# Optimization experiments

Measured on AMD Instinct MI355X. Metric: run time of the kernel, lower is better.

The kernel has to match this reference:

```python
import jax, jax.numpy as jnp
import numpy as np

B, CTX, QST, E, H = 8, 4096, 512, 300, 128

def setup_inputs() -> dict:
    key = jax.random.key(0)
    k1, k2, k3, k4 = jax.random.split(key, 4)
    context_sequence = jax.random.normal(k1, (B, CTX, E), dtype=jnp.float32)
    question_sequence = jax.random.normal(k2, (B, QST, E), dtype=jnp.float32)
    question_mask = jnp.ones((B, QST), dtype=jnp.int32)
    # dense layer params (PyTorch Linear: y = x @ W.T + b)
    bound = 1.0 / np.sqrt(E)
    W = jax.random.uniform(k3, (H, E), minval=-bound, maxval=bound, dtype=jnp.float32)
    b = jax.random.uniform(k4, (H,), minval=-bound, maxval=bound, dtype=jnp.float32)
    return {"context_sequence": context_sequence, "question_sequence": question_sequence,
            "question_mask": question_mask, "W": W, "b": b}

def reference(context_sequence, question_sequence, question_mask, W, b):
    # ReLU(dense(x)) for both sequences
    ctx_logits = jax.nn.relu(jnp.einsum('bce,he->bch', context_sequence, W) + b)   # [B, CTX, H]
    qst_logits = jax.nn.relu(jnp.einsum('bqe,he->bqh', question_sequence, W) + b)  # [B, QST, H]
    scores = jnp.einsum('bch,bqh->bcq', ctx_logits, qst_logits)                    # [B, CTX, QST]
    scores = jnp.where(question_mask[:, None, :] == 0, -jnp.inf, scores)
    attn = jax.nn.softmax(scores, axis=-1)
    return jnp.einsum('bcq,bqh->bch', attn, qst_logits)                            # [B, CTX, H]
```

## Files before the change

kernel.cpp:

```cpp
#include <hip/hip_runtime.h>
#include <hip/hip_bf16.h>

#define BB   8
#define SCTX 4096
#define SQ   512
#define EE   300
#define HH   128
#define EP   320
#define CST  328
#define LOG2E 1.4426950408889634f

typedef short bhalf4 __attribute__((ext_vector_type(4)));
typedef short short8 __attribute__((ext_vector_type(8)));
typedef float f32x4  __attribute__((ext_vector_type(4)));
typedef unsigned u32x4 __attribute__((ext_vector_type(4)));

#define MFMA16(a, b, c) __builtin_amdgcn_mfma_f32_16x16x32_bf16((a), (b), (c), 0, 0, 0)

__device__ __forceinline__ short f2bf(float f) {
  unsigned u = __builtin_bit_cast(unsigned, f);
  u += 0x7fffu + ((u >> 16) & 1u);
  return (short)(u >> 16);
}
__device__ __forceinline__ float bf2f(short s) {
  return __builtin_bit_cast(float, ((unsigned)(unsigned short)s) << 16);
}
__device__ __forceinline__ unsigned pack2(float a, float b) {
  return (unsigned)(unsigned short)f2bf(a) | ((unsigned)(unsigned short)f2bf(b) << 16);
}
__device__ __forceinline__ void gload16(const void* g, void* lds) {
  __builtin_amdgcn_global_load_lds(
      (const __attribute__((address_space(1))) void*)g,
      (__attribute__((address_space(3))) void*)lds, 16, 0, 0);
}

__global__ void k_wpad(const float* __restrict__ W, short* __restrict__ wsw) {
  const int h = blockIdx.x, k = threadIdx.x;
  float v = (k < EE) ? W[h * EE + k] : 0.0f;
  const int m = h >> 4, t = h & 15, kk = k >> 5, quad = (k >> 3) & 3, j = k & 7;
  wsw[((kk * 8 + m) * 64 + quad * 16 + t) * 8 + j] = f2bf(v);
}

__global__ __launch_bounds__(256) void k_qlog(const float* __restrict__ qst,
                                              const short* __restrict__ wsw,
                                              const float* __restrict__ bias,
                                              short* __restrict__ ql,
                                              short* __restrict__ qlT) {
  const int b = blockIdx.y;
  const int m0 = blockIdx.x * 32;
  const int tid = threadIdx.x;
  const int w = tid >> 6, l = tid & 63, t = l & 15, quad = l >> 4;
  const int g = w >> 1, hf = w & 1;

  __shared__ __align__(16) short cst[32 * CST];

  const float4* cbase = (const float4*)(qst + (size_t)(b * SQ + m0) * EE);
#pragma unroll
  for (int j = 0; j < 10; ++j) {
    int i4 = tid + j * 256;
    if (i4 < 2400) {
      float4 v = cbase[i4];
      int row = i4 / 75, c4 = i4 - row * 75;
      bhalf4 s4; s4[0] = f2bf(v.x); s4[1] = f2bf(v.y); s4[2] = f2bf(v.z); s4[3] = f2bf(v.w);
      *(bhalf4*)(cst + row * CST + c4 * 4) = s4;
    }
  }
  for (int i = tid; i < 320; i += 256) {
    int row = i / 10, c = (i - row * 10) * 2;
    *(int*)&cst[row * CST + 300 + c] = 0;
  }
  __syncthreads();

  const short* arow = cst + (g * 16 + t) * CST;
  f32x4 acc[4] = {};
#pragma unroll
  for (int kk = 0; kk < 10; ++kk) {
    const int k = kk * 32 + quad * 8;
    short8 a = *(const short8*)(arow + k);
    short8 w8[4];
#pragma unroll
    for (int n = 0; n < 4; ++n)
      w8[n] = *(const short8*)(wsw + ((kk * 8 + hf * 4 + n) * 64 + l) * 8);
#pragma unroll
    for (int n = 0; n < 4; ++n) acc[n] = MFMA16(a, w8[n], acc[n]);
  }
#pragma unroll
  for (int n = 0; n < 4; ++n) {
    const int h = (hf * 4 + n) * 16 + t;
    const float bv = bias[h];
    bhalf4 s4;
#pragma unroll
    for (int r = 0; r < 4; ++r) {
      float v = fmaxf(acc[n][r] + bv, 0.0f);
      short s16 = f2bf(v);
      s4[r] = s16;
      const int row = m0 + g * 16 + quad * 4 + r;
      ql[((size_t)b * SQ + row) * HH + h] = s16;
    }
    *(bhalf4*)&qlT[((size_t)b * HH + h) * SQ + m0 + g * 16 + quad * 4] = s4;
  }
}

__global__ __launch_bounds__(256, 2) void k_attn(const float* __restrict__ ctx,
                                                 const short* __restrict__ wsw,
                                                 const float* __restrict__ bias,
                                                 const int* __restrict__ mask,
                                                 const short* __restrict__ ql,
                                                 const short* __restrict__ qlT,
                                                 float* __restrict__ out) {
  const int b = blockIdx.y;
  const int m0 = blockIdx.x * 64;
  const int tid = threadIdx.x;
  const int w = tid >> 6, l = tid & 63, t = l & 15, quad = l >> 4;
  const int g = w >> 1, hf = w & 1;

  __shared__ __align__(16) short uq[16384];
  __shared__ __align__(16) short uv[16384];
  __shared__ short maskh[SQ];
  short* cst = uq;
  short* qch = uq;
  short* clt = uv;
  short* vch = uv;

  for (int i = tid; i < SQ; i += 256)
    maskh[i] = f2bf(mask[b * SQ + i] ? -8.0f : -1e30f);

  for (int i = 0; i < 2; ++i) {
    const float4* cbase = (const float4*)(ctx + ((size_t)b * SCTX + m0 + i * 32) * EE);
#pragma unroll
    for (int j = 0; j < 10; ++j) {
      int i4 = tid + j * 256;
      if (i4 < 2400) {
        float4 v = cbase[i4];
        int row = i4 / 75, c4 = i4 - row * 75;
        bhalf4 s4; s4[0] = f2bf(v.x); s4[1] = f2bf(v.y); s4[2] = f2bf(v.z); s4[3] = f2bf(v.w);
        *(bhalf4*)(cst + row * CST + c4 * 4) = s4;
      }
    }
    for (int k = tid; k < 320; k += 256) {
      int row = k / 10, c = (k - row * 10) * 2;
      *(int*)&cst[row * CST + 300 + c] = 0;
    }
    __syncthreads();
    const short* arow = cst + (g * 16 + t) * CST;
    f32x4 acc[4] = {};
#pragma unroll
    for (int kk = 0; kk < 10; ++kk) {
      const int k = kk * 32 + quad * 8;
      short8 a = *(const short8*)(arow + k);
      short8 w8[4];
#pragma unroll
      for (int n = 0; n < 4; ++n)
        w8[n] = *(const short8*)(wsw + ((kk * 8 + hf * 4 + n) * 64 + l) * 8);
#pragma unroll
      for (int n = 0; n < 4; ++n) acc[n] = MFMA16(a, w8[n], acc[n]);
    }
#pragma unroll
    for (int n = 0; n < 4; ++n) {
      const int h = (hf * 4 + n) * 16 + t;
      const float bv = bias[h];
#pragma unroll
      for (int r = 0; r < 4; ++r) {
        float v = fmaxf(acc[n][r] + bv, 0.0f);
        clt[(i * 32 + g * 16 + quad * 4 + r) * 136 + h] = f2bf(v);
      }
    }
    __syncthreads();
  }

  short8 af[4];
#pragma unroll
  for (int kk = 0; kk < 4; ++kk)
    af[kk] = *(const short8*)&clt[(w * 16 + t) * 136 + kk * 32 + quad * 8];

  const int srcA = ((quad & 1) * 2) * 16 + t;
  const int srcB = srcA + 16;
  const bool hiq = quad >= 2;
  const int sx = (t & 7) << 3;
  const int rl = l >> 4;
  const int cb = (l & 15) * 16;

  auto stageQ = [&](int c) {
#pragma unroll
    for (int s = 0; s < 8; ++s) {
      const int row = w * 32 + s * 4 + rl;
      const int sw = cb ^ ((row & 7) << 4);
      gload16((const char*)(ql + ((size_t)b * SQ + c * 128 + row) * HH) + sw,
              qch + (w * 32 + s * 4) * 128);
    }
  };
  auto stageV = [&](int c) {
#pragma unroll
    for (int s = 0; s < 8; ++s) {
      const int row = w * 32 + s * 4 + rl;
      const int sw = cb ^ ((row & 7) << 4);
      gload16((const char*)(qlT + ((size_t)b * HH + row) * SQ + c * 128) + sw,
              vch + (w * 32 + s * 4) * 128);
    }
  };

  stageQ(0);

  f32x4 o[8] = {};
  float rtot = 0.0f;
  for (int c = 0; c < 4; ++c) {
    __syncthreads();
    stageV(c);

    f32x4 sv[8] = {};
#pragma unroll
    for (int kk = 0; kk < 4; ++kk) {
      const short* qrE = qch + ((kk * 2) * 16 + t) * 128;
      const short* qrO = qrE + 16 * 128;
#pragma unroll
      for (int kx = 0; kx < 4; ++kx) {
        const int co = (kx * 32 + quad * 8) ^ sx;
        sv[kk * 2]     = MFMA16(*(const short8*)(qrE + co), af[kx], sv[kk * 2]);
        sv[kk * 2 + 1] = MFMA16(*(const short8*)(qrO + co), af[kx], sv[kk * 2 + 1]);
      }
    }
    unsigned pk[16];
#pragma unroll
    for (int kk = 0; kk < 4; ++kk) {
      bhalf4 mbE = *(const bhalf4*)&maskh[c * 128 + (kk * 2) * 16 + quad * 4];
      bhalf4 mbO = *(const bhalf4*)&maskh[c * 128 + (kk * 2 + 1) * 16 + quad * 4];
      float pE[4], pO[4];
#pragma unroll
      for (int r = 0; r < 4; ++r) {
        pE[r] = exp2f((sv[kk * 2][r] + bf2f(mbE[r])) * LOG2E);
        pO[r] = exp2f((sv[kk * 2 + 1][r] + bf2f(mbO[r])) * LOG2E);
        rtot += pE[r] + pO[r];
      }
      pk[kk * 4 + 0] = pack2(pE[0], pE[1]);
      pk[kk * 4 + 1] = pack2(pE[2], pE[3]);
      pk[kk * 4 + 2] = pack2(pO[0], pO[1]);
      pk[kk * 4 + 3] = pack2(pO[2], pO[3]);
    }
    unsigned sA[16], sB[16];
#pragma unroll
    for (int i = 0; i < 16; ++i) {
      sA[i] = (unsigned)__shfl((int)pk[i], srcA);
      sB[i] = (unsigned)__shfl((int)pk[i], srcB);
    }

    __syncthreads();

    if (c < 3) stageQ(c + 1);

#pragma unroll
    for (int kk = 0; kk < 4; ++kk) {
      u32x4 av;
      av[0] = hiq ? sA[kk * 4 + 2] : sA[kk * 4 + 0];
      av[1] = hiq ? sA[kk * 4 + 3] : sA[kk * 4 + 1];
      av[2] = hiq ? sB[kk * 4 + 2] : sB[kk * 4 + 0];
      av[3] = hiq ? sB[kk * 4 + 3] : sB[kk * 4 + 1];
      short8 pa = __builtin_bit_cast(short8, av);
      const int co = (kk * 32 + quad * 8) ^ sx;
#pragma unroll
      for (int n = 0; n < 8; ++n) {
        short8 v8 = *(const short8*)&vch[(n * 16 + t) * 128 + co];
        o[n] = MFMA16(pa, v8, o[n]);
      }
    }
  }

  rtot += __shfl_xor(rtot, 16);
  rtot += __shfl_xor(rtot, 32);
  f32x4 rinv;
#pragma unroll
  for (int r = 0; r < 4; ++r) rinv[r] = 1.0f / __shfl(rtot, quad * 4 + r);
  float* obase = out + ((size_t)b * SCTX + m0 + w * 16) * HH;
#pragma unroll
  for (int n = 0; n < 8; ++n)
#pragma unroll
    for (int r = 0; r < 4; ++r)
      obase[(quad * 4 + r) * HH + n * 16 + t] = o[n][r] * rinv[r];
}

extern "C" void kernel_launch(void* const* d_in, const int* in_sizes, int n_in,
                              void* d_out, int out_size, void* d_ws, size_t ws_size,
                              hipStream_t stream) {
  const float* ctx  = (const float*)d_in[0];
  const float* qst  = (const float*)d_in[1];
  const int*   mask = (const int*)d_in[2];
  const float* W    = (const float*)d_in[3];
  const float* bias = (const float*)d_in[4];
  float* out = (float*)d_out;

  short* wsw  = (short*)d_ws;
  short* ql   = (short*)((char*)d_ws + 81920);
  short* qlT  = ql + (size_t)BB * SQ * HH;

  k_wpad<<<dim3(HH), dim3(EP), 0, stream>>>(W, wsw);
  k_qlog<<<dim3(SQ / 32, BB), dim3(256), 0, stream>>>(qst, wsw, bias, ql, qlT);
  k_attn<<<dim3(SCTX / 64, BB), dim3(256), 0, stream>>>(ctx, wsw, bias, mask, ql, qlT, out);
}
```

Measured before the change: 121.1 us.

## Halve attention tile to 32 rows and split question keys across warps

```diff
diff --git a/kernel.cpp b/kernel.cpp
--- a/kernel.cpp
+++ b/kernel.cpp
@@ -8,6 +8,7 @@
 #define HH   128
 #define EP   320
 #define CST  328
+#define CSH  168
 #define LOG2E 1.4426950408889634f
 
 typedef short bhalf4 __attribute__((ext_vector_type(4)));
@@ -109,172 +110,193 @@
                                                  const short* __restrict__ qlT,
                                                  float* __restrict__ out) {
   const int b = blockIdx.y;
-  const int m0 = blockIdx.x * 64;
+  const int m0 = blockIdx.x * 32;
   const int tid = threadIdx.x;
   const int w = tid >> 6, l = tid & 63, t = l & 15, quad = l >> 4;
-  const int g = w >> 1, hf = w & 1;
-
-  __shared__ __align__(16) short uq[16384];
-  __shared__ __align__(16) short uv[16384];
-  __shared__ short maskh[SQ];
-  short* cst = uq;
+  const int rg = w & 1, qh = w >> 1;
+
+  __shared__ __align__(16) short uq[8192];
+  __shared__ __align__(16) short uv[8192];
+  __shared__ __align__(16) short maskh[SQ];
   short* qch = uq;
-  short* clt = uv;
+  short* csth = uv;
   short* vch = uv;
+
+  const int rl4 = l >> 4;
+  const int cbq = (l & 15) * 16;
+  const int rl8 = l >> 3;
+  const int cbv = (l & 7) * 16;
+
+  auto stageQ = [&](int c) {
+#pragma unroll
+    for (int s = 0; s < 4; ++s) {
+      const int row = w * 16 + s * 4 + rl4;
+      gload16((const char*)(ql + ((size_t)b * SQ + c * 64 + row) * HH) +
+                  (cbq ^ ((row & 7) << 4)),
+              qch + (w * 16 + s * 4) * 128);
+    }
+  };
+  auto stageV = [&](int c) {
+#pragma unroll
+    for (int s = 0; s < 4; ++s) {
+      const int row = w * 32 + s * 8 + rl8;
+      gload16((const char*)(qlT + ((size_t)b * HH + row) * SQ + c * 64) +
+                  (cbv ^ ((row & 7) << 4)),
+              vch + (w * 32 + s * 8) * 64);
+    }
+  };
+
+  stageQ(0);
 
   for (int i = tid; i < SQ; i += 256)
     maskh[i] = f2bf(mask[b * SQ + i] ? -8.0f : -1e30f);
 
-  for (int i = 0; i < 2; ++i) {
-    const float4* cbase = (const float4*)(ctx + ((size_t)b * SCTX + m0 + i * 32) * EE);
-#pragma unroll
-    for (int j = 0; j < 10; ++j) {
-      int i4 = tid + j * 256;
-      if (i4 < 2400) {
-        float4 v = cbase[i4];
-        int row = i4 / 75, c4 = i4 - row * 75;
+  f32x4 acc[8] = {};
+  for (int kh = 0; kh < 2; ++kh) {
+    if (kh == 0) {
+#pragma unroll
+      for (int j = 0; j < 5; ++j) {
+        int i4 = tid + j * 256;
+        int row = i4 / 40, c4 = i4 - row * 40;
+        float4 v = *(const float4*)(ctx + ((size_t)b * SCTX + m0 + row) * EE + c4 * 4);
         bhalf4 s4; s4[0] = f2bf(v.x); s4[1] = f2bf(v.y); s4[2] = f2bf(v.z); s4[3] = f2bf(v.w);
-        *(bhalf4*)(cst + row * CST + c4 * 4) = s4;
-      }
-    }
-    for (int k = tid; k < 320; k += 256) {
-      int row = k / 10, c = (k - row * 10) * 2;
-      *(int*)&cst[row * CST + 300 + c] = 0;
+        *(bhalf4*)(csth + row * CSH + c4 * 4) = s4;
+      }
+    } else {
+#pragma unroll
+      for (int j = 0; j < 5; ++j) {
+        int i4 = tid + j * 256;
+        if (i4 < 1120) {
+          int row = i4 / 35, c4 = i4 - row * 35;
+          float4 v = *(const float4*)(ctx + ((size_t)b * SCTX + m0 + row) * EE + 160 + c4 * 4);
+          bhalf4 s4; s4[0] = f2bf(v.x); s4[1] = f2bf(v.y); s4[2] = f2bf(v.z); s4[3] = f2bf(v.w);
+          *(bhalf4*)(csth + row * CSH + c4 * 4) = s4;
+        }
+      }
+      for (int i = tid; i < 320; i += 256) {
+        int row = i / 10, ci = (i - row * 10) * 2;
+        *(int*)&csth[row * CSH + 140 + ci] = 0;
+      }
     }
     __syncthreads();
-    const short* arow = cst + (g * 16 + t) * CST;
-    f32x4 acc[4] = {};
-#pragma unroll
-    for (int kk = 0; kk < 10; ++kk) {
-      const int k = kk * 32 + quad * 8;
-      short8 a = *(const short8*)(arow + k);
-      short8 w8[4];
-#pragma unroll
-      for (int n = 0; n < 4; ++n)
-        w8[n] = *(const short8*)(wsw + ((kk * 8 + hf * 4 + n) * 64 + l) * 8);
-#pragma unroll
-      for (int n = 0; n < 4; ++n) acc[n] = MFMA16(a, w8[n], acc[n]);
-    }
-#pragma unroll
-    for (int n = 0; n < 4; ++n) {
-      const int h = (hf * 4 + n) * 16 + t;
-      const float bv = bias[h];
-#pragma unroll
-      for (int r = 0; r < 4; ++r) {
-        float v = fmaxf(acc[n][r] + bv, 0.0f);
-        clt[(i * 32 + g * 16 + quad * 4 + r) * 136 + h] = f2bf(v);
+    const short* arow = csth + (rg * 16 + t) * CSH;
+#pragma unroll
+    for (int kkl = 0; kkl < 5; ++kkl) {
+      const int kk = kh * 5 + kkl;
+      short8 a = *(const short8*)(arow + kkl * 32 + quad * 8);
+#pragma unroll
+      for (int n = 0; n < 8; ++n) {
+        short8 w8 = *(const short8*)(wsw + ((kk * 8 + n) * 64 + l) * 8);
+        acc[n] = MFMA16(w8, a, acc[n]);
       }
     }
     __syncthreads();
   }
-
-  short8 af[4];
-#pragma unroll
-  for (int kk = 0; kk < 4; ++kk)
-    af[kk] = *(const short8*)&clt[(w * 16 + t) * 136 + kk * 32 + quad * 8];
 
   const int srcA = ((quad & 1) * 2) * 16 + t;
   const int srcB = srcA + 16;
   const bool hiq = quad >= 2;
+  unsigned pkA[8][2];
+#pragma unroll
+  for (int n = 0; n < 8; ++n) {
+    float4 bv = *(const float4*)(bias + n * 16 + quad * 4);
+    pkA[n][0] = pack2(fmaxf(acc[n][0] + bv.x, 0.f), fmaxf(acc[n][1] + bv.y, 0.f));
+    pkA[n][1] = pack2(fmaxf(acc[n][2] + bv.z, 0.f), fmaxf(acc[n][3] + bv.w, 0.f));
+  }
+  short8 af[4];
+#pragma unroll
+  for (int kk = 0; kk < 4; ++kk) {
+    unsigned e0 = (unsigned)__shfl((int)pkA[kk * 2][0], srcA);
+    unsigned e1 = (unsigned)__shfl((int)pkA[kk * 2][1], srcA);
+    unsigned e2 = (unsigned)__shfl((int)pkA[kk * 2][0], srcB);
+    unsigned e3 = (unsigned)__shfl((int)pkA[kk * 2][1], srcB);
+    unsigned o0 = (unsigned)__shfl((int)pkA[kk * 2 + 1][0], srcA);
+    unsigned o1 = (unsigned)__shfl((int)pkA[kk * 2 + 1][1], srcA);
+    unsigned o2 = (unsigned)__shfl((int)pkA[kk * 2 + 1][0], srcB);
+    unsigned o3 = (unsigned)__shfl((int)pkA[kk * 2 + 1][1], srcB);
+    u32x4 a4;
+    a4[0] = hiq ? o0 : e0;
+    a4[1] = hiq ? o1 : e1;
+    a4[2] = hiq ? o2 : e2;
+    a4[3] = hiq ? o3 : e3;
+    af[kk] = __builtin_bit_cast(short8, a4);
+  }
+
   const int sx = (t & 7) << 3;
-  const int rl = l >> 4;
-  const int cb = (l & 15) * 16;
-
-  auto stageQ = [&](int c) {
-#pragma unroll
-    for (int s = 0; s < 8; ++s) {
-      const int row = w * 32 + s * 4 + rl;
-      const int sw = cb ^ ((row & 7) << 4);
-      gload16((const char*)(ql + ((size_t)b * SQ + c * 128 + row) * HH) + sw,
-              qch + (w * 32 + s * 4) * 128);
-    }
-  };
-  auto stageV = [&](int c) {
-#pragma unroll
-    for (int s = 0; s < 8; ++s) {
-      const int row = w * 32 + s * 4 + rl;
-      const int sw = cb ^ ((row & 7) << 4);
-      gload16((const char*)(qlT + ((size_t)b * HH + row) * SQ + c * 128) + sw,
-              vch + (w * 32 + s * 4) * 128);
-    }
-  };
-
-  stageQ(0);
-
   f32x4 o[8] = {};
   float rtot = 0.0f;
-  for (int c = 0; c < 4; ++c) {
+  for (int c = 0; c < 8; ++c) {
     __syncthreads();
     stageV(c);
-
-    f32x4 sv[8] = {};
-#pragma unroll
-    for (int kk = 0; kk < 4; ++kk) {
-      const short* qrE = qch + ((kk * 2) * 16 + t) * 128;
-      const short* qrO = qrE + 16 * 128;
+    f32x4 sv[2] = {};
+#pragma unroll
+    for (int n2 = 0; n2 < 2; ++n2) {
+      const short* qr = qch + (qh * 32 + n2 * 16 + t) * 128;
 #pragma unroll
       for (int kx = 0; kx < 4; ++kx) {
-        const int co = (kx * 32 + quad * 8) ^ sx;
-        sv[kk * 2]     = MFMA16(*(const short8*)(qrE + co), af[kx], sv[kk * 2]);
-        sv[kk * 2 + 1] = MFMA16(*(const short8*)(qrO + co), af[kx], sv[kk * 2 + 1]);
-      }
-    }
-    unsigned pk[16];
-#pragma unroll
-    for (int kk = 0; kk < 4; ++kk) {
-      bhalf4 mbE = *(const bhalf4*)&maskh[c * 128 + (kk * 2) * 16 + quad * 4];
-      bhalf4 mbO = *(const bhalf4*)&maskh[c * 128 + (kk * 2 + 1) * 16 + quad * 4];
-      float pE[4], pO[4];
-#pragma unroll
-      for (int r = 0; r < 4; ++r) {
-        pE[r] = exp2f((sv[kk * 2][r] + bf2f(mbE[r])) * LOG2E);
-        pO[r] = exp2f((sv[kk * 2 + 1][r] + bf2f(mbO[r])) * LOG2E);
-        rtot += pE[r] + pO[r];
-      }
-      pk[kk * 4 + 0] = pack2(pE[0], pE[1]);
-      pk[kk * 4 + 1] = pack2(pE[2], pE[3]);
-      pk[kk * 4 + 2] = pack2(pO[0], pO[1]);
-      pk[kk * 4 + 3] = pack2(pO[2], pO[3]);
-    }
-    unsigned sA[16], sB[16];
-#pragma unroll
-    for (int i = 0; i < 16; ++i) {
+        short8 b8 = *(const short8*)(qr + ((kx * 32 + quad * 8) ^ sx));
+        sv[n2] = MFMA16(b8, af[kx], sv[n2]);
+      }
+    }
+    unsigned pk[4];
+#pragma unroll
+    for (int n2 = 0; n2 < 2; ++n2) {
+      bhalf4 mb = *(const bhalf4*)&maskh[c * 64 + qh * 32 + n2 * 16 + quad * 4];
+      float p0 = exp2f((sv[n2][0] + bf2f(mb[0])) * LOG2E);
+      float p1 = exp2f((sv[n2][1] + bf2f(mb[1])) * LOG2E);
+      float p2 = exp2f((sv[n2][2] + bf2f(mb[2])) * LOG2E);
+      float p3 = exp2f((sv[n2][3] + bf2f(mb[3])) * LOG2E);
+      rtot += (p0 + p1) + (p2 + p3);
+      pk[n2 * 2 + 0] = pack2(p0, p1);
+      pk[n2 * 2 + 1] = pack2(p2, p3);
+    }
+    unsigned sA[4], sB[4];
+#pragma unroll
+    for (int i = 0; i < 4; ++i) {
       sA[i] = (unsigned)__shfl((int)pk[i], srcA);
       sB[i] = (unsigned)__shfl((int)pk[i], srcB);
     }
-
     __syncthreads();
-
-    if (c < 3) stageQ(c + 1);
-
-#pragma unroll
-    for (int kk = 0; kk < 4; ++kk) {
-      u32x4 av;
-      av[0] = hiq ? sA[kk * 4 + 2] : sA[kk * 4 + 0];
-      av[1] = hiq ? sA[kk * 4 + 3] : sA[kk * 4 + 1];
-      av[2] = hiq ? sB[kk * 4 + 2] : sB[kk * 4 + 0];
-      av[3] = hiq ? sB[kk * 4 + 3] : sB[kk * 4 + 1];
-      short8 pa = __builtin_bit_cast(short8, av);
-      const int co = (kk * 32 + quad * 8) ^ sx;
-#pragma unroll
-      for (int n = 0; n < 8; ++n) {
-        short8 v8 = *(const short8*)&vch[(n * 16 + t) * 128 + co];
-        o[n] = MFMA16(pa, v8, o[n]);
-      }
-    }
-  }
-
-  rtot += __shfl_xor(rtot, 16);
-  rtot += __shfl_xor(rtot, 32);
-  f32x4 rinv;
-#pragma unroll
-  for (int r = 0; r < 4; ++r) rinv[r] = 1.0f / __shfl(rtot, quad * 4 + r);
-  float* obase = out + ((size_t)b * SCTX + m0 + w * 16) * HH;
-#pragma unroll
-  for (int n = 0; n < 8; ++n)
-#pragma unroll
-    for (int r = 0; r < 4; ++r)
-      obase[(quad * 4 + r) * HH + n * 16 + t] = o[n][r] * rinv[r];
+    if (c < 7) stageQ(c + 1);
+    u32x4 av;
+    av[0] = hiq ? sA[2] : sA[0];
+    av[1] = hiq ? sA[3] : sA[1];
+    av[2] = hiq ? sB[2] : sB[0];
+    av[3] = hiq ? sB[3] : sB[1];
+    short8 pa = __builtin_bit_cast(short8, av);
+#pragma unroll
+    for (int n = 0; n < 8; ++n) {
+      short8 v8 = *(const short8*)&vch[(n * 16 + t) * 64 + ((qh * 32 + quad * 8) ^ sx)];
+      o[n] = MFMA16(pa, v8, o[n]);
+    }
+  }
+
+  float* obuf = (float*)uq;
+  float* rbuf = (float*)maskh;
+  if (qh == 1) {
+#pragma unroll
+    for (int n = 0; n < 8; ++n)
+      *(f32x4*)&obuf[rg * 2048 + n * 256 + l * 4] = o[n];
+    rbuf[rg * 64 + l] = rtot;
+  }
+  __syncthreads();
+  if (qh == 0) {
+    rtot += rbuf[rg * 64 + l];
+#pragma unroll
+    for (int n = 0; n < 8; ++n)
+      o[n] += *(const f32x4*)&obuf[rg * 2048 + n * 256 + l * 4];
+    rtot += __shfl_xor(rtot, 16);
+    rtot += __shfl_xor(rtot, 32);
+    f32x4 rinv;
+#pragma unroll
+    for (int r = 0; r < 4; ++r) rinv[r] = 1.0f / __shfl(rtot, quad * 4 + r);
+    float* obase = out + ((size_t)b * SCTX + m0 + rg * 16) * HH;
+#pragma unroll
+    for (int n = 0; n < 8; ++n)
+#pragma unroll
+      for (int r = 0; r < 4; ++r)
+        obase[(quad * 4 + r) * HH + n * 16 + t] = o[n][r] * rinv[r];
+  }
 }
 
 extern "C" void kernel_launch(void* const* d_in, const int* in_sizes, int n_in,
@@ -293,5 +315,5 @@
 
   k_wpad<<<dim3(HH), dim3(EP), 0, stream>>>(W, wsw);
   k_qlog<<<dim3(SQ / 32, BB), dim3(256), 0, stream>>>(qst, wsw, bias, ql, qlT);
-  k_attn<<<dim3(SCTX / 64, BB), dim3(256), 0, stream>>>(ctx, wsw, bias, mask, ql, qlT, out);
-}
+  k_attn<<<dim3(SCTX / 32, BB), dim3(256), 0, stream>>>(ctx, wsw, bias, mask, ql, qlT, out);
+}
```

Result: slower. 131.6 us (+8.7%).

## Double-buffer Q and V chunks with 64-wide tiles and manual vmcnt waits

Applied to the files above, without the earlier changes.

```diff
diff --git a/kernel.cpp b/kernel.cpp
--- a/kernel.cpp
+++ b/kernel.cpp
@@ -16,6 +16,8 @@
 typedef unsigned u32x4 __attribute__((ext_vector_type(4)));
 
 #define MFMA16(a, b, c) __builtin_amdgcn_mfma_f32_16x16x32_bf16((a), (b), (c), 0, 0, 0)
+#define SBAR()   __builtin_amdgcn_s_barrier()
+#define SCHED0() __builtin_amdgcn_sched_barrier(0)
 
 __device__ __forceinline__ short f2bf(float f) {
   unsigned u = __builtin_bit_cast(unsigned, f);
@@ -116,11 +118,11 @@
 
   __shared__ __align__(16) short uq[16384];
   __shared__ __align__(16) short uv[16384];
-  __shared__ short maskh[SQ];
+  __shared__ __align__(16) short maskh[SQ];
   short* cst = uq;
-  short* qch = uq;
   short* clt = uv;
-  short* vch = uv;
+  short* qb0 = uq;          short* qb1 = uq + 8192;
+  short* vb0 = uv;          short* vb1 = uv + 8192;
 
   for (int i = tid; i < SQ; i += 256)
     maskh[i] = f2bf(mask[b * SQ + i] ? -8.0f : -1e30f);
@@ -172,95 +174,93 @@
 #pragma unroll
   for (int kk = 0; kk < 4; ++kk)
     af[kk] = *(const short8*)&clt[(w * 16 + t) * 136 + kk * 32 + quad * 8];
+  __syncthreads();
 
   const int srcA = ((quad & 1) * 2) * 16 + t;
   const int srcB = srcA + 16;
   const bool hiq = quad >= 2;
-  const int sx = (t & 7) << 3;
-  const int rl = l >> 4;
-  const int cb = (l & 15) * 16;
-
-  auto stageQ = [&](int c) {
-#pragma unroll
-    for (int s = 0; s < 8; ++s) {
-      const int row = w * 32 + s * 4 + rl;
-      const int sw = cb ^ ((row & 7) << 4);
-      gload16((const char*)(ql + ((size_t)b * SQ + c * 128 + row) * HH) + sw,
-              qch + (w * 32 + s * 4) * 128);
+  const int sx  = (t & 7) << 3;
+  const int rl4 = l >> 4;
+  const int cbq = (l & 15) * 16;
+  const int rl8 = l >> 3;
+  const int cbv = (l & 7) * 16;
+
+  auto stageTo = [&](short* qb, short* vb, int c) {
+#pragma unroll
+    for (int s = 0; s < 4; ++s) {
+      const int row = w * 16 + s * 4 + rl4;
+      gload16((const char*)(ql + ((size_t)b * SQ + c * 64 + row) * HH) +
+                  (cbq ^ ((row & 7) << 4)),
+              qb + (w * 16 + s * 4) * 128);
+    }
+#pragma unroll
+    for (int s = 0; s < 4; ++s) {
+      const int row = w * 32 + s * 8 + rl8;
+      gload16((const char*)(qlT + ((size_t)b * HH + row) * SQ + c * 64) +
+                  (cbv ^ ((row & 7) << 4)),
+              vb + (w * 32 + s * 8) * 64);
     }
   };
-  auto stageV = [&](int c) {
-#pragma unroll
-    for (int s = 0; s < 8; ++s) {
-      const int row = w * 32 + s * 4 + rl;
-      const int sw = cb ^ ((row & 7) << 4);
-      gload16((const char*)(qlT + ((size_t)b * HH + row) * SQ + c * 128) + sw,
-              vch + (w * 32 + s * 4) * 128);
-    }
-  };
-
-  stageQ(0);
+
+  stageTo(qb0, vb0, 0);
+  stageTo(qb1, vb1, 1);
 
   f32x4 o[8] = {};
   float rtot = 0.0f;
-  for (int c = 0; c < 4; ++c) {
-    __syncthreads();
-    stageV(c);
-
-    f32x4 sv[8] = {};
-#pragma unroll
-    for (int kk = 0; kk < 4; ++kk) {
-      const short* qrE = qch + ((kk * 2) * 16 + t) * 128;
-      const short* qrO = qrE + 16 * 128;
+  for (int c = 0; c < 8; ++c) {
+    short* qch = (c & 1) ? qb1 : qb0;
+    short* vch = (c & 1) ? vb1 : vb0;
+    if (c < 7) { asm volatile("s_waitcnt vmcnt(8)" ::: "memory"); }
+    else       { asm volatile("s_waitcnt vmcnt(0)" ::: "memory"); }
+    SCHED0(); SBAR(); SCHED0();
+
+    f32x4 sv[4] = {};
+#pragma unroll
+    for (int n2 = 0; n2 < 4; ++n2) {
+      const short* qr = qch + (n2 * 16 + t) * 128;
 #pragma unroll
       for (int kx = 0; kx < 4; ++kx) {
-        const int co = (kx * 32 + quad * 8) ^ sx;
-        sv[kk * 2]     = MFMA16(*(const short8*)(qrE + co), af[kx], sv[kk * 2]);
-        sv[kk * 2 + 1] = MFMA16(*(const short8*)(qrO + co), af[kx], sv[kk * 2 + 1]);
-      }
-    }
-    unsigned pk[16];
-#pragma unroll
-    for (int kk = 0; kk < 4; ++kk) {
-      bhalf4 mbE = *(const bhalf4*)&maskh[c * 128 + (kk * 2) * 16 + quad * 4];
-      bhalf4 mbO = *(const bhalf4*)&maskh[c * 128 + (kk * 2 + 1) * 16 + quad * 4];
-      float pE[4], pO[4];
-#pragma unroll
-      for (int r = 0; r < 4; ++r) {
-        pE[r] = exp2f((sv[kk * 2][r] + bf2f(mbE[r])) * LOG2E);
-        pO[r] = exp2f((sv[kk * 2 + 1][r] + bf2f(mbO[r])) * LOG2E);
-        rtot += pE[r] + pO[r];
-      }
-      pk[kk * 4 + 0] = pack2(pE[0], pE[1]);
-      pk[kk * 4 + 1] = pack2(pE[2], pE[3]);
-      pk[kk * 4 + 2] = pack2(pO[0], pO[1]);
-      pk[kk * 4 + 3] = pack2(pO[2], pO[3]);
-    }
-    unsigned sA[16], sB[16];
-#pragma unroll
-    for (int i = 0; i < 16; ++i) {
+        short8 b8 = *(const short8*)(qr + ((kx * 32 + quad * 8) ^ sx));
+        sv[n2] = MFMA16(b8, af[kx], sv[n2]);
+      }
+    }
+    unsigned pk[8];
+#pragma unroll
+    for (int n2 = 0; n2 < 4; ++n2) {
+      bhalf4 mb = *(const bhalf4*)&maskh[c * 64 + n2 * 16 + quad * 4];
+      float p0 = exp2f((sv[n2][0] + bf2f(mb[0])) * LOG2E);
+      float p1 = exp2f((sv[n2][1] + bf2f(mb[1])) * LOG2E);
+      float p2 = exp2f((sv[n2][2] + bf2f(mb[2])) * LOG2E);
+      float p3 = exp2f((sv[n2][3] + bf2f(mb[3])) * LOG2E);
+      rtot += (p0 + p1) + (p2 + p3);
+      pk[n2 * 2 + 0] = pack2(p0, p1);
+      pk[n2 * 2 + 1] = pack2(p2, p3);
+    }
+    unsigned sA[8], sB[8];
+#pragma unroll
+    for (int i = 0; i < 8; ++i) {
       sA[i] = (unsigned)__shfl((int)pk[i], srcA);
       sB[i] = (unsigned)__shfl((int)pk[i], srcB);
     }
-
-    __syncthreads();
-
-    if (c < 3) stageQ(c + 1);
-
-#pragma unroll
-    for (int kk = 0; kk < 4; ++kk) {
+#pragma unroll
+    for (int kk2 = 0; kk2 < 2; ++kk2) {
       u32x4 av;
-      av[0] = hiq ? sA[kk * 4 + 2] : sA[kk * 4 + 0];
-      av[1] = hiq ? sA[kk * 4 + 3] : sA[kk * 4 + 1];
-      av[2] = hiq ? sB[kk * 4 + 2] : sB[kk * 4 + 0];
-      av[3] = hiq ? sB[kk * 4 + 3] : sB[kk * 4 + 1];
+      av[0] = hiq ? sA[kk2 * 4 + 2] : sA[kk2 * 4 + 0];
+      av[1] = hiq ? sA[kk2 * 4 + 3] : sA[kk2 * 4 + 1];
+      av[2] = hiq ? sB[kk2 * 4 + 2] : sB[kk2 * 4 + 0];
+      av[3] = hiq ? sB[kk2 * 4 + 3] : sB[kk2 * 4 + 1];
       short8 pa = __builtin_bit_cast(short8, av);
-      const int co = (kk * 32 + quad * 8) ^ sx;
+      const int co = (kk2 * 32 + quad * 8) ^ sx;
 #pragma unroll
       for (int n = 0; n < 8; ++n) {
-        short8 v8 = *(const short8*)&vch[(n * 16 + t) * 128 + co];
+        short8 v8 = *(const short8*)&vch[(n * 16 + t) * 64 + co];
         o[n] = MFMA16(pa, v8, o[n]);
       }
+    }
+    if (c < 7) {
+      asm volatile("s_waitcnt lgkmcnt(0)" ::: "memory");
+      SCHED0(); SBAR(); SCHED0();
+      if (c < 6) stageTo(qch, vch, c + 2);
     }
   }
 
```

Result: no change. 121.2 us (+0.0%).
